# Kernel tuning notes

Measured on AMD Instinct MI355X. Metric: run time of the kernel, lower is better.

## Reference

```python
import jax, jax.numpy as jnp
import numpy as np

B, L, D = 2, 4096, 128      # batch, seq_len, d_model
ED = 2 * D                  # d_inner (expand=2) = 256
N = 16                      # d_state
K = 4                       # d_conv
R = (D + 15) // 16          # dt_rank = 8
H = 2 * D                   # mlp hidden = 256


def setup_inputs() -> dict:
    key = jax.random.key(0)
    ks = jax.random.split(key, 20)
    s = 0.05
    inp = {
        "x": jax.random.normal(ks[0], (B, L, D), dtype=jnp.float32),
        # outer block LayerNorm (norm1)
        "norm1_g": jnp.ones((D,), jnp.float32),
        "norm1_b": jnp.zeros((D,), jnp.float32),
        # MambaLayer inner LayerNorm
        "inner_g": jnp.ones((D,), jnp.float32),
        "inner_b": jnp.zeros((D,), jnp.float32),
        # Mamba params
        "in_w": jax.random.normal(ks[1], (2 * ED, D), jnp.float32) * s,      # in_proj (no bias)
        "conv_w": jax.random.normal(ks[2], (ED, 1, K), jnp.float32) * s,     # depthwise conv
        "conv_b": jax.random.normal(ks[3], (ED,), jnp.float32) * s,
        "xproj_w": jax.random.normal(ks[4], (R + 2 * N, ED), jnp.float32) * s,  # x_proj (no bias)
        "dt_w": jax.random.normal(ks[5], (ED, R), jnp.float32) * s,
        "dt_b": jax.random.normal(ks[6], (ED,), jnp.float32) * s,
        "A_log": jnp.tile(jnp.log(jnp.arange(1, N + 1, dtype=jnp.float32)), (ED, 1)),  # [ED,N]
        "Dp": jnp.ones((ED,), jnp.float32),
        "out_w": jax.random.normal(ks[7], (D, ED), jnp.float32) * s,         # out_proj (no bias)
        # MLP
        "fc1_w": jax.random.normal(ks[8], (H, D), jnp.float32) * s,
        "fc1_b": jnp.zeros((H,), jnp.float32),
        "fc2_w": jax.random.normal(ks[9], (D, H), jnp.float32) * s,
        "fc2_b": jnp.zeros((D,), jnp.float32),
    }
    return inp


def _ln(x, g, b, eps=1e-5):
    m = jnp.mean(x, axis=-1, keepdims=True)
    v = jnp.mean((x - m) ** 2, axis=-1, keepdims=True)
    return (x - m) * jax.lax.rsqrt(v + eps) * g + b


def _mamba(x, in_w, conv_w, conv_b, xproj_w, dt_w, dt_b, A_log, Dp, out_w):
    # x: [B, L, D]
    xz = jnp.einsum('bld,ed->ble', x, in_w)          # [B,L,2*ED]
    u, z = jnp.split(xz, 2, axis=-1)                 # each [B,L,ED]
    # causal depthwise conv1d over L
    u_c = jnp.transpose(u, (0, 2, 1))                # [B,ED,L]
    u_c = jax.lax.conv_general_dilated(
        u_c, conv_w, window_strides=(1,), padding=[(K - 1, 0)],
        dimension_numbers=('NCH', 'OIH', 'NCH'), feature_group_count=ED)
    u = jax.nn.silu(jnp.transpose(u_c, (0, 2, 1)) + conv_b)   # [B,L,ED]
    # input-dependent dt, B, C
    dbc = jnp.einsum('ble,re->blr', u, xproj_w)      # [B,L,R+2N]
    dt, Bm, Cm = jnp.split(dbc, [R, R + N], axis=-1)
    delta = jax.nn.softplus(jnp.einsum('blr,er->ble', dt, dt_w) + dt_b)  # [B,L,ED]
    A = -jnp.exp(A_log)                              # [ED,N]
    deltaA = jnp.exp(jnp.einsum('ble,en->blen', delta, A))               # [B,L,ED,N]
    deltaBu = jnp.einsum('ble,bln,ble->blen', delta, Bm, u)              # [B,L,ED,N]
    # selective scan over L
    def step(h, inp):
        dA, dBu, Ct = inp                            # [B,ED,N],[B,ED,N],[B,N]
        h = dA * h + dBu
        y = jnp.einsum('ben,bn->be', h, Ct)
        return h, y
    h0 = jnp.zeros((B, ED, N), u.dtype)
    xs = (jnp.transpose(deltaA, (1, 0, 2, 3)),
          jnp.transpose(deltaBu, (1, 0, 2, 3)),
          jnp.transpose(Cm, (1, 0, 2)))
    _, ys = jax.lax.scan(step, h0, xs)               # [L,B,ED]
    y = jnp.transpose(ys, (1, 0, 2)) + u * Dp        # [B,L,ED]
    y = y * jax.nn.silu(z)
    return jnp.einsum('ble,de->bld', y, out_w)       # [B,L,D]


def reference(x, norm1_g, norm1_b, inner_g, inner_b, in_w, conv_w, conv_b,
              xproj_w, dt_w, dt_b, A_log, Dp, out_w, fc1_w, fc1_b, fc2_w, fc2_b):
    # attn branch: mamba(inner_LN(norm1(x)))
    a = _mamba(_ln(_ln(x, norm1_g, norm1_b), inner_g, inner_b),
               in_w, conv_w, conv_b, xproj_w, dt_w, dt_b, A_log, Dp, out_w)
    x = x + a
    # mlp branch (note: original applies norm1 again to updated x)
    h = _ln(x, norm1_g, norm1_b)
    h = jax.nn.gelu(jnp.einsum('bld,hd->blh', h, fc1_w) + fc1_b, approximate=False)
    h = jnp.einsum('blh,dh->bld', h, fc2_w) + fc2_b
    return x + h
```

## Files before the change

kernel.cpp:

```cpp
#include <hip/hip_runtime.h>
#include <hip/hip_bf16.h>
#include <math.h>

#define BB 2
#define LL 4096
#define DD 128
#define ED 256
#define NN 16
#define KK 4
#define RR 8
#define HH 256
#define NT (BB*LL)
#define NC 128
#define LC 32

typedef __attribute__((ext_vector_type(8))) short short8;
typedef __attribute__((ext_vector_type(8))) unsigned short ushort8v;
typedef __attribute__((ext_vector_type(4))) float floatx4;

__device__ __forceinline__ unsigned short f2bf(float f) {
  unsigned int b = __builtin_bit_cast(unsigned int, f);
  b += 0x7FFFu + ((b >> 16) & 1u);
  return (unsigned short)(b >> 16);
}

__global__ __launch_bounds__(256) void cvt5_k(const float* __restrict__ a,
    const float* __restrict__ b, const float* __restrict__ c,
    const float* __restrict__ d, const float* __restrict__ e5,
    unsigned short* __restrict__ oa, unsigned short* __restrict__ ob,
    unsigned short* __restrict__ oc, unsigned short* __restrict__ od,
    unsigned short* __restrict__ oe) {
  const int i = blockIdx.x*256 + threadIdx.x;
  const float* src; unsigned short* dst; int off;
  if (i < 16384)      { src = a;  dst = oa; off = i; }
  else if (i < 24576) { src = b;  dst = ob; off = i - 16384; }
  else if (i < 32768) { src = c;  dst = oc; off = i - 24576; }
  else if (i < 40960) { src = d;  dst = od; off = i - 32768; }
  else                { src = e5; dst = oe; off = i - 40960; }
  const float4 v = ((const float4*)src)[off];
  unsigned int lo = f2bf(v.x) | ((unsigned int)f2bf(v.y) << 16);
  unsigned int hi = f2bf(v.z) | ((unsigned int)f2bf(v.w) << 16);
  ((uint2*)dst)[off] = make_uint2(lo, hi);
}

template<bool DOUBLE>
__global__ __launch_bounds__(256) void ln2_k(const float* __restrict__ x,
    const float* __restrict__ g1, const float* __restrict__ b1,
    const float* __restrict__ g2, const float* __restrict__ b2,
    unsigned short* __restrict__ out) {
  const int token = blockIdx.x*4 + (threadIdx.x >> 6);
  const int lane  = threadIdx.x & 63;
  float2 v = *(const float2*)(x + (size_t)token*DD + lane*2);

  auto wsum = [&](float s) -> float {
    s += __shfl_xor(s, 32); s += __shfl_xor(s, 16); s += __shfl_xor(s, 8);
    s += __shfl_xor(s, 4);  s += __shfl_xor(s, 2);  s += __shfl_xor(s, 1);
    return s;
  };

  float mean = wsum(v.x + v.y) * (1.f/128.f);
  float cx = v.x - mean, cy = v.y - mean;
  float var = wsum(cx*cx + cy*cy) * (1.f/128.f);
  float rs = rsqrtf(var + 1e-5f);
  const float2 g = *(const float2*)(g1 + lane*2);
  const float2 bb = *(const float2*)(b1 + lane*2);
  float yx = cx*rs*g.x + bb.x;
  float yy = cy*rs*g.y + bb.y;
  if constexpr (DOUBLE) {
    float m2 = wsum(yx + yy) * (1.f/128.f);
    float c2x = yx - m2, c2y = yy - m2;
    float v2 = wsum(c2x*c2x + c2y*c2y) * (1.f/128.f);
    float rs2 = rsqrtf(v2 + 1e-5f);
    const float2 g2v = *(const float2*)(g2 + lane*2);
    const float2 b2v = *(const float2*)(b2 + lane*2);
    yx = c2x*rs2*g2v.x + b2v.x;
    yy = c2y*rs2*g2v.y + b2v.y;
  }
  const unsigned int packed = f2bf(yx) | ((unsigned int)f2bf(yy) << 16);
  *(unsigned int*)(out + (size_t)token*DD + lane*2) = packed;
}

template<int KD, int EPI, typename OT>
__global__ __launch_bounds__(256) void gemm_bf_k(
    const unsigned short* __restrict__ A, const unsigned short* __restrict__ W,
    const float* __restrict__ bias, const float* __restrict__ res,
    OT* __restrict__ C, int Nn) {
  static_assert(KD % 128 == 0, "KD multiple of 128");
  __shared__ unsigned short As[64][136];
  __shared__ unsigned short Ws[64][136];

  const int row0 = blockIdx.y * 64;
  const int col0 = blockIdx.x * 64;
  const int tid  = threadIdx.x;
  const int wave = tid >> 6;
  const int lane = tid & 63;
  const int quad = lane >> 4;
  const int l16  = lane & 15;
  const int wm = (wave & 1) * 32;
  const int wn = (wave >> 1) * 32;
  const int lr = tid >> 2;
  const int lc = (tid & 3) * 32;

  floatx4 acc[2][2] = {};

  for (int ks0 = 0; ks0 < KD; ks0 += 128) {
    const unsigned short* Ap = A + (size_t)(row0 + lr)*KD + ks0 + lc;
    const unsigned short* Wp = W + (size_t)(col0 + lr)*KD + ks0 + lc;
    ushort8v av[4], wv[4];
    #pragma unroll
    for (int g = 0; g < 4; g++) {
      av[g] = *(const ushort8v*)(Ap + g*8);
      wv[g] = *(const ushort8v*)(Wp + g*8);
    }
    __syncthreads();
    #pragma unroll
    for (int g = 0; g < 4; g++) {
      *(ushort8v*)&As[lr][lc + g*8] = av[g];
      *(ushort8v*)&Ws[lr][lc + g*8] = wv[g];
    }
    __syncthreads();
    #pragma unroll
    for (int ks = 0; ks < 4; ks++) {
      const int ko = ks*32 + quad*8;
      short8 a0 = *(const short8*)&As[wm +      l16][ko];
      short8 a1 = *(const short8*)&As[wm + 16 + l16][ko];
      short8 b0 = *(const short8*)&Ws[wn +      l16][ko];
      short8 b1 = *(const short8*)&Ws[wn + 16 + l16][ko];
      acc[0][0] = __builtin_amdgcn_mfma_f32_16x16x32_bf16(a0, b0, acc[0][0], 0, 0, 0);
      acc[0][1] = __builtin_amdgcn_mfma_f32_16x16x32_bf16(a0, b1, acc[0][1], 0, 0, 0);
      acc[1][0] = __builtin_amdgcn_mfma_f32_16x16x32_bf16(a1, b0, acc[1][0], 0, 0, 0);
      acc[1][1] = __builtin_amdgcn_mfma_f32_16x16x32_bf16(a1, b1, acc[1][1], 0, 0, 0);
    }
  }

  #pragma unroll
  for (int i = 0; i < 2; i++) {
    #pragma unroll
    for (int j = 0; j < 2; j++) {
      const int n = col0 + wn + j*16 + l16;
      float bn = 0.f;
      if constexpr (EPI == 2 || EPI == 3) bn = bias[n];
      #pragma unroll
      for (int r = 0; r < 4; r++) {
        const int m = row0 + wm + i*16 + quad*4 + r;
        float v = acc[i][j][r];
        if constexpr (EPI == 2 || EPI == 3) v += bn;
        if constexpr (EPI == 2) v = 0.5f*v*(1.f + erff(v*0.70710678118f));
        const size_t o = (size_t)m*Nn + n;
        if constexpr (EPI == 1 || EPI == 3) v += res[o];
        if constexpr (sizeof(OT) == 2) C[o] = (OT)f2bf(v);
        else                           C[o] = v;
      }
    }
  }
}

__global__ __launch_bounds__(256) void mamba_mid_k(const float* __restrict__ xz,
    const float* __restrict__ cw, const float* __restrict__ cb,
    const unsigned short* __restrict__ xpwb, const float* __restrict__ dtw,
    const float* __restrict__ dtb, float* __restrict__ uc,
    float* __restrict__ dbc, float* __restrict__ delta) {
  __shared__ unsigned short As[32][264];
  __shared__ unsigned short Bs[64][264];
  __shared__ float sd[32][8];
  const int t0  = blockIdx.x * 32;
  const int tid = threadIdx.x;

  #pragma unroll
  for (int p = 0; p < 8; p++) {
    const int idx = p*256 + tid;
    const int row = idx >> 5;
    const int col = (idx & 31) * 8;
    ushort8v v = {};
    if (row < 40) v = *(const ushort8v*)(xpwb + row*ED + col);
    *(ushort8v*)&Bs[row][col] = v;
  }

  const int e = tid;
  const float4 w = *(const float4*)(cw + e*4);
  const float cbe = cb[e];
  float h0 = 0.f, h1 = 0.f, h2 = 0.f;
  if (t0 & 4095) {
    h0 = xz[(size_t)(t0-3)*(2*ED) + e];
    h1 = xz[(size_t)(t0-2)*(2*ED) + e];
    h2 = xz[(size_t)(t0-1)*(2*ED) + e];
  }
  #pragma unroll 4
  for (int i = 0; i < 32; i++) {
    const float cur = xz[(size_t)(t0+i)*(2*ED) + e];
    const float a = cbe + h0*w.x + h1*w.y + h2*w.z + cur*w.w;
    const float s = a / (1.f + __expf(-a));
    As[i][e] = f2bf(s);
    uc[(size_t)(t0+i)*ED + e] = s;
    h0 = h1; h1 = h2; h2 = cur;
  }
  __syncthreads();

  const int wave = tid >> 6, lane = tid & 63;
  const int quad = lane >> 4, l16 = lane & 15;
  const int mi = (wave & 1) * 16;
  const int j0 = (wave >> 1) * 2;
  floatx4 acc[2] = {};
  #pragma unroll
  for (int ks = 0; ks < 8; ks++) {
    const int ko = ks*32 + quad*8;
    short8 a  = *(const short8*)&As[mi + l16][ko];
    short8 b0 = *(const short8*)&Bs[j0*16 +      l16][ko];
    short8 b1 = *(const short8*)&Bs[j0*16 + 16 + l16][ko];
    acc[0] = __builtin_amdgcn_mfma_f32_16x16x32_bf16(a, b0, acc[0], 0, 0, 0);
    acc[1] = __builtin_amdgcn_mfma_f32_16x16x32_bf16(a, b1, acc[1], 0, 0, 0);
  }
  #pragma unroll
  for (int f = 0; f < 2; f++) {
    const int n = (j0 + f)*16 + l16;
    #pragma unroll
    for (int r = 0; r < 4; r++) {
      const int m = mi + quad*4 + r;
      const float v = acc[f][r];
      if (n < 40) dbc[(size_t)(t0 + m)*40 + n] = v;
      if (n < RR) sd[m][n] = v;
    }
  }
  __syncthreads();

  const float4 w0 = *(const float4*)(dtw + e*RR);
  const float4 w1 = *(const float4*)(dtw + e*RR + 4);
  const float db = dtb[e];
  #pragma unroll 4
  for (int t = 0; t < 32; t++) {
    const float a = db
        + sd[t][0]*w0.x + sd[t][1]*w0.y + sd[t][2]*w0.z + sd[t][3]*w0.w
        + sd[t][4]*w1.x + sd[t][5]*w1.y + sd[t][6]*w1.z + sd[t][7]*w1.w;
    delta[(size_t)(t0+t)*ED + e] = (a > 20.f) ? a : log1pf(__expf(a));
  }
}

__global__ __launch_bounds__(256) void scan1_k(const float* __restrict__ delta,
    const float* __restrict__ uc, const float* __restrict__ dbc,
    const float* __restrict__ A_log, float* __restrict__ cA,
    float* __restrict__ cH) {
  const int c = blockIdx.y, b = blockIdx.z;
  const int e  = blockIdx.x*128 + (threadIdx.x >> 1);
  const int n0 = (threadIdx.x & 1) * 8;
  const float4 a0 = *(const float4*)(A_log + e*NN + n0);
  const float4 a1 = *(const float4*)(A_log + e*NN + n0 + 4);
  float Aen[8] = {-__expf(a0.x), -__expf(a0.y), -__expf(a0.z), -__expf(a0.w),
                  -__expf(a1.x), -__expf(a1.y), -__expf(a1.z), -__expf(a1.w)};
  float h[8] = {};
  float sumd = 0.f;
  const size_t tok0 = (size_t)b*LL + (size_t)c*LC;
  for (int i = 0; i < LC; i++) {
    const size_t t = tok0 + i;
    const float dv = delta[t*ED + e];
    const float uv = uc[t*ED + e];
    const float du = dv * uv;
    const float4 B0 = *(const float4*)(dbc + t*40 + RR + n0);
    const float4 B1 = *(const float4*)(dbc + t*40 + RR + n0 + 4);
    const float Bv[8] = {B0.x,B0.y,B0.z,B0.w,B1.x,B1.y,B1.z,B1.w};
    sumd += dv;
    #pragma unroll
    for (int j = 0; j < 8; j++) {
      const float dA = __expf(dv * Aen[j]);
      h[j] = dA*h[j] + Bv[j]*du;
    }
  }
  const size_t base = (((size_t)c*BB + b)*ED + e)*NN + n0;
  *(float4*)(cA + base)     = make_float4(__expf(sumd*Aen[0]), __expf(sumd*Aen[1]),
                                          __expf(sumd*Aen[2]), __expf(sumd*Aen[3]));
  *(float4*)(cA + base + 4) = make_float4(__expf(sumd*Aen[4]), __expf(sumd*Aen[5]),
                                          __expf(sumd*Aen[6]), __expf(sumd*Aen[7]));
  *(float4*)(cH + base)     = make_float4(h[0], h[1], h[2], h[3]);
  *(float4*)(cH + base + 4) = make_float4(h[4], h[5], h[6], h[7]);
}

__global__ __launch_bounds__(256) void scan2_k(float* __restrict__ cA,
    const float* __restrict__ cH) {
  const int gt = blockIdx.x*256 + threadIdx.x;
  const int b = gt >> 12;
  const size_t base = (size_t)b*ED*NN + (gt & 4095);
  float h = 0.f;
  for (int c = 0; c < NC; c++) {
    const size_t idx = (size_t)c*(BB*ED*NN) + base;
    const float a = cA[idx], hh = cH[idx];
    cA[idx] = h;
    h = a*h + hh;
  }
}

__global__ __launch_bounds__(256) void scan3_k(const float* __restrict__ delta,
    const float* __restrict__ uc, const float* __restrict__ dbc,
    const float* __restrict__ xz, const float* __restrict__ A_log,
    const float* __restrict__ Dpv, const float* __restrict__ cP,
    unsigned short* __restrict__ ybf) {
  const int c = blockIdx.y, b = blockIdx.z;
  const int e    = blockIdx.x*128 + (threadIdx.x >> 1);
  const int half = threadIdx.x & 1;
  const int n0   = half * 8;
  const float4 a0 = *(const float4*)(A_log + e*NN + n0);
  const float4 a1 = *(const float4*)(A_log + e*NN + n0 + 4);
  float Aen[8] = {-__expf(a0.x), -__expf(a0.y), -__expf(a0.z), -__expf(a0.w),
                  -__expf(a1.x), -__expf(a1.y), -__expf(a1.z), -__expf(a1.w)};
  const float Dpe = Dpv[e];
  const size_t base = (((size_t)c*BB + b)*ED + e)*NN + n0;
  const float4 h0 = *(const float4*)(cP + base);
  const float4 h1 = *(const float4*)(cP + base + 4);
  float h[8] = {h0.x,h0.y,h0.z,h0.w,h1.x,h1.y,h1.z,h1.w};
  const size_t tok0 = (size_t)b*LL + (size_t)c*LC;
  for (int i = 0; i < LC; i++) {
    const size_t t = tok0 + i;
    const float dv = delta[t*ED + e];
    const float uv = uc[t*ED + e];
    const float du = dv * uv;
    const float4 B0 = *(const float4*)(dbc + t*40 + RR + n0);
    const float4 B1 = *(const float4*)(dbc + t*40 + RR + n0 + 4);
    const float4 C0 = *(const float4*)(dbc + t*40 + RR + NN + n0);
    const float4 C1 = *(const float4*)(dbc + t*40 + RR + NN + n0 + 4);
    const float Bv[8] = {B0.x,B0.y,B0.z,B0.w,B1.x,B1.y,B1.z,B1.w};
    const float Cv[8] = {C0.x,C0.y,C0.z,C0.w,C1.x,C1.y,C1.z,C1.w};
    float part = 0.f;
    #pragma unroll
    for (int j = 0; j < 8; j++) {
      const float dA = __expf(dv * Aen[j]);
      h[j] = dA*h[j] + Bv[j]*du;
      part += h[j]*Cv[j];
    }
    part += __shfl_xor(part, 1);
    if (half == 0) {
      const float zv = xz[t*(2*ED) + ED + e];
      const float g = zv / (1.f + __expf(-zv));
      ybf[t*ED + e] = f2bf((part + uv*Dpe) * g);
    }
  }
}

extern "C" void kernel_launch(void* const* d_in, const int* in_sizes, int n_in,
                              void* d_out, int out_size, void* d_ws, size_t ws_size,
                              hipStream_t stream) {
  const float* x      = (const float*)d_in[0];
  const float* n1g    = (const float*)d_in[1];
  const float* n1b    = (const float*)d_in[2];
  const float* ing    = (const float*)d_in[3];
  const float* inb    = (const float*)d_in[4];
  const float* in_w   = (const float*)d_in[5];
  const float* conv_w = (const float*)d_in[6];
  const float* conv_b = (const float*)d_in[7];
  const float* xproj_w= (const float*)d_in[8];
  const float* dt_w   = (const float*)d_in[9];
  const float* dt_b   = (const float*)d_in[10];
  const float* A_log  = (const float*)d_in[11];
  const float* Dpv    = (const float*)d_in[12];
  const float* out_w  = (const float*)d_in[13];
  const float* fc1_w  = (const float*)d_in[14];
  const float* fc1_b  = (const float*)d_in[15];
  const float* fc2_w  = (const float*)d_in[16];
  const float* fc2_b  = (const float*)d_in[17];
  float* out = (float*)d_out;

  float* ws    = (float*)d_ws;
  float* xz    = ws;
  float* uc    = xz    + (size_t)NT*2*ED;
  float* dbc   = uc    + (size_t)NT*ED;
  float* delta = dbc   + (size_t)NT*40;
  float* cAP   = delta + (size_t)NT*ED;
  float* cH    = cAP   + (size_t)NC*BB*ED*NN;
  float* xnew  = cH    + (size_t)NC*BB*ED*NN;
  unsigned short* xnbf  = (unsigned short*)(xnew + (size_t)NT*DD);
  unsigned short* ybf   = xnbf  + (size_t)NT*DD;
  unsigned short* hlnbf = ybf   + (size_t)NT*ED;
  unsigned short* hmlbf = hlnbf + (size_t)NT*DD;
  unsigned short* wbin  = hmlbf + (size_t)NT*HH;
  unsigned short* wbout = wbin  + (size_t)2*ED*DD;
  unsigned short* wbf1  = wbout + (size_t)DD*ED;
  unsigned short* wbf2  = wbf1  + (size_t)HH*DD;
  unsigned short* wbxp  = wbf2  + (size_t)DD*HH;

  cvt5_k<<<170, 256, 0, stream>>>(in_w, out_w, fc1_w, fc2_w, xproj_w,
                                  wbin, wbout, wbf1, wbf2, wbxp);
  ln2_k<true><<<NT/4, 256, 0, stream>>>(x, n1g, n1b, ing, inb, xnbf);
  gemm_bf_k<DD,0,float><<<dim3(512/64, NT/64), 256, 0, stream>>>(xnbf, wbin, nullptr, nullptr, xz, 2*ED);
  mamba_mid_k<<<NT/32, 256, 0, stream>>>(xz, conv_w, conv_b, wbxp, dt_w, dt_b, uc, dbc, delta);
  scan1_k<<<dim3(2, NC, BB), 256, 0, stream>>>(delta, uc, dbc, A_log, cAP, cH);
  scan2_k<<<(BB*ED*NN)/256, 256, 0, stream>>>(cAP, cH);
  scan3_k<<<dim3(2, NC, BB), 256, 0, stream>>>(delta, uc, dbc, xz, A_log, Dpv, cAP, ybf);
  gemm_bf_k<ED,1,float><<<dim3(DD/64, NT/64), 256, 0, stream>>>(ybf, wbout, nullptr, x, xnew, DD);
  ln2_k<false><<<NT/4, 256, 0, stream>>>(xnew, n1g, n1b, nullptr, nullptr, hlnbf);
  gemm_bf_k<DD,2,unsigned short><<<dim3(HH/64, NT/64), 256, 0, stream>>>(hlnbf, wbf1, fc1_b, nullptr, hmlbf, HH);
  gemm_bf_k<HH,3,float><<<dim3(DD/64, NT/64), 256, 0, stream>>>(hmlbf, wbf2, fc2_b, xnew, out, DD);
}
```

Baseline: 189.1 us.

## Fuse conv, x_proj, dt and three scan phases into one cooperative kernel

Merges the conv/x_proj/dt kernel and the three chunked-scan kernels into a single cooperative kernel that uses grid.sync between the chunk-local scan, the cross-chunk prefix and the final output pass. The conv output, delta and B/C values stay in shared memory, so the uc, dbc and delta workspace tensors are no longer written to and reread from global memory. The cross-chunk pass also batches its loads in groups of 16 to expose more memory parallelism. In exchange, each block recomputes the conv for all 256 channels, because the x_proj GEMM needs them even though the block scans only 128. The design also depends on all 512 blocks being co-resident, and the two grid-wide barriers add cost.

```diff
diff --git a/kernel.cpp b/kernel.cpp
--- a/kernel.cpp
+++ b/kernel.cpp
@@ -1,5 +1,6 @@
 #include <hip/hip_runtime.h>
 #include <hip/hip_bf16.h>
+#include <hip/hip_cooperative_groups.h>
 #include <math.h>
 
 #define BB 2
@@ -155,16 +156,28 @@
   }
 }
 
-__global__ __launch_bounds__(256) void mamba_mid_k(const float* __restrict__ xz,
-    const float* __restrict__ cw, const float* __restrict__ cb,
-    const unsigned short* __restrict__ xpwb, const float* __restrict__ dtw,
-    const float* __restrict__ dtb, float* __restrict__ uc,
-    float* __restrict__ dbc, float* __restrict__ delta) {
-  __shared__ unsigned short As[32][264];
-  __shared__ unsigned short Bs[64][264];
-  __shared__ float sd[32][8];
-  const int t0  = blockIdx.x * 32;
+__global__ __launch_bounds__(256) void mamba_core_k(
+    const float* __restrict__ xz, const float* __restrict__ cw,
+    const float* __restrict__ cb, const unsigned short* __restrict__ xpwb,
+    const float* __restrict__ dtw, const float* __restrict__ dtb,
+    const float* __restrict__ A_log, const float* __restrict__ Dpv,
+    float* __restrict__ cA, float* __restrict__ cH,
+    unsigned short* __restrict__ ybf) {
+  namespace cg = cooperative_groups;
+  cg::grid_group grid = cg::this_grid();
+
+  __shared__ __align__(16) unsigned short Bs[64][264];
+  __shared__ __align__(16) unsigned short As[32][264];
+  __shared__ float su[32][128];
+  __shared__ float sdbc[32][40];
+  float (*sdel)[128] = reinterpret_cast<float(*)[128]>(&As[0][0]);
+
+  const int gid = blockIdx.x;
+  const int eb = gid & 1;
+  const int b  = (gid >> 1) & 1;
+  const int c  = gid >> 2;
   const int tid = threadIdx.x;
+  const int t0 = b*LL + c*LC;
 
   #pragma unroll
   for (int p = 0; p < 8; p++) {
@@ -176,159 +189,154 @@
     *(ushort8v*)&Bs[row][col] = v;
   }
 
-  const int e = tid;
-  const float4 w = *(const float4*)(cw + e*4);
-  const float cbe = cb[e];
-  float h0 = 0.f, h1 = 0.f, h2 = 0.f;
-  if (t0 & 4095) {
-    h0 = xz[(size_t)(t0-3)*(2*ED) + e];
-    h1 = xz[(size_t)(t0-2)*(2*ED) + e];
-    h2 = xz[(size_t)(t0-1)*(2*ED) + e];
-  }
-  #pragma unroll 4
-  for (int i = 0; i < 32; i++) {
-    const float cur = xz[(size_t)(t0+i)*(2*ED) + e];
-    const float a = cbe + h0*w.x + h1*w.y + h2*w.z + cur*w.w;
-    const float s = a / (1.f + __expf(-a));
-    As[i][e] = f2bf(s);
-    uc[(size_t)(t0+i)*ED + e] = s;
-    h0 = h1; h1 = h2; h2 = cur;
+  {
+    const int ch = tid;
+    const float4 w = *(const float4*)(cw + ch*4);
+    const float cbe = cb[ch];
+    float h0 = 0.f, h1 = 0.f, h2 = 0.f;
+    if (c != 0) {
+      h0 = xz[(size_t)(t0-3)*(2*ED) + ch];
+      h1 = xz[(size_t)(t0-2)*(2*ED) + ch];
+      h2 = xz[(size_t)(t0-1)*(2*ED) + ch];
+    }
+    const bool own = (ch >> 7) == eb;
+    #pragma unroll 8
+    for (int i = 0; i < LC; i++) {
+      const float cur = xz[(size_t)(t0+i)*(2*ED) + ch];
+      const float a = cbe + h0*w.x + h1*w.y + h2*w.z + cur*w.w;
+      const float s = a / (1.f + __expf(-a));
+      As[i][ch] = f2bf(s);
+      if (own) su[i][ch & 127] = s;
+      h0 = h1; h1 = h2; h2 = cur;
+    }
   }
   __syncthreads();
 
   const int wave = tid >> 6, lane = tid & 63;
   const int quad = lane >> 4, l16 = lane & 15;
-  const int mi = (wave & 1) * 16;
-  const int j0 = (wave >> 1) * 2;
-  floatx4 acc[2] = {};
-  #pragma unroll
-  for (int ks = 0; ks < 8; ks++) {
-    const int ko = ks*32 + quad*8;
-    short8 a  = *(const short8*)&As[mi + l16][ko];
-    short8 b0 = *(const short8*)&Bs[j0*16 +      l16][ko];
-    short8 b1 = *(const short8*)&Bs[j0*16 + 16 + l16][ko];
-    acc[0] = __builtin_amdgcn_mfma_f32_16x16x32_bf16(a, b0, acc[0], 0, 0, 0);
-    acc[1] = __builtin_amdgcn_mfma_f32_16x16x32_bf16(a, b1, acc[1], 0, 0, 0);
-  }
-  #pragma unroll
-  for (int f = 0; f < 2; f++) {
-    const int n = (j0 + f)*16 + l16;
-    #pragma unroll
-    for (int r = 0; r < 4; r++) {
-      const int m = mi + quad*4 + r;
-      const float v = acc[f][r];
-      if (n < 40) dbc[(size_t)(t0 + m)*40 + n] = v;
-      if (n < RR) sd[m][n] = v;
+  {
+    const int mi = (wave & 1) * 16;
+    const int j0 = (wave >> 1) * 2;
+    floatx4 acc[2] = {};
+    #pragma unroll
+    for (int ks = 0; ks < 8; ks++) {
+      const int ko = ks*32 + quad*8;
+      short8 a  = *(const short8*)&As[mi + l16][ko];
+      short8 b0 = *(const short8*)&Bs[j0*16 +      l16][ko];
+      short8 b1 = *(const short8*)&Bs[j0*16 + 16 + l16][ko];
+      acc[0] = __builtin_amdgcn_mfma_f32_16x16x32_bf16(a, b0, acc[0], 0, 0, 0);
+      acc[1] = __builtin_amdgcn_mfma_f32_16x16x32_bf16(a, b1, acc[1], 0, 0, 0);
+    }
+    __syncthreads();
+    #pragma unroll
+    for (int f = 0; f < 2; f++) {
+      const int n = (j0 + f)*16 + l16;
+      #pragma unroll
+      for (int r = 0; r < 4; r++) {
+        const int m = mi + quad*4 + r;
+        if (n < 40) sdbc[m][n] = acc[f][r];
+      }
     }
   }
   __syncthreads();
 
-  const float4 w0 = *(const float4*)(dtw + e*RR);
-  const float4 w1 = *(const float4*)(dtw + e*RR + 4);
-  const float db = dtb[e];
-  #pragma unroll 4
-  for (int t = 0; t < 32; t++) {
-    const float a = db
-        + sd[t][0]*w0.x + sd[t][1]*w0.y + sd[t][2]*w0.z + sd[t][3]*w0.w
-        + sd[t][4]*w1.x + sd[t][5]*w1.y + sd[t][6]*w1.z + sd[t][7]*w1.w;
-    delta[(size_t)(t0+t)*ED + e] = (a > 20.f) ? a : log1pf(__expf(a));
-  }
-}
-
-__global__ __launch_bounds__(256) void scan1_k(const float* __restrict__ delta,
-    const float* __restrict__ uc, const float* __restrict__ dbc,
-    const float* __restrict__ A_log, float* __restrict__ cA,
-    float* __restrict__ cH) {
-  const int c = blockIdx.y, b = blockIdx.z;
-  const int e  = blockIdx.x*128 + (threadIdx.x >> 1);
-  const int n0 = (threadIdx.x & 1) * 8;
+  const int e_loc = tid >> 1;
+  const int half  = tid & 1;
+  const int e     = eb*128 + e_loc;
+  {
+    const float4 w0 = *(const float4*)(dtw + e*RR);
+    const float4 w1 = *(const float4*)(dtw + e*RR + 4);
+    const float db = dtb[e];
+    #pragma unroll 4
+    for (int i = 0; i < 16; i++) {
+      const int t = half*16 + i;
+      const float a = db
+          + sdbc[t][0]*w0.x + sdbc[t][1]*w0.y + sdbc[t][2]*w0.z + sdbc[t][3]*w0.w
+          + sdbc[t][4]*w1.x + sdbc[t][5]*w1.y + sdbc[t][6]*w1.z + sdbc[t][7]*w1.w;
+      sdel[t][e_loc] = (a > 20.f) ? a : log1pf(__expf(a));
+    }
+  }
+  __syncthreads();
+
+  const int n0 = half * 8;
   const float4 a0 = *(const float4*)(A_log + e*NN + n0);
   const float4 a1 = *(const float4*)(A_log + e*NN + n0 + 4);
   float Aen[8] = {-__expf(a0.x), -__expf(a0.y), -__expf(a0.z), -__expf(a0.w),
                   -__expf(a1.x), -__expf(a1.y), -__expf(a1.z), -__expf(a1.w)};
-  float h[8] = {};
-  float sumd = 0.f;
-  const size_t tok0 = (size_t)b*LL + (size_t)c*LC;
-  for (int i = 0; i < LC; i++) {
-    const size_t t = tok0 + i;
-    const float dv = delta[t*ED + e];
-    const float uv = uc[t*ED + e];
-    const float du = dv * uv;
-    const float4 B0 = *(const float4*)(dbc + t*40 + RR + n0);
-    const float4 B1 = *(const float4*)(dbc + t*40 + RR + n0 + 4);
-    const float Bv[8] = {B0.x,B0.y,B0.z,B0.w,B1.x,B1.y,B1.z,B1.w};
-    sumd += dv;
-    #pragma unroll
-    for (int j = 0; j < 8; j++) {
-      const float dA = __expf(dv * Aen[j]);
-      h[j] = dA*h[j] + Bv[j]*du;
-    }
-  }
   const size_t base = (((size_t)c*BB + b)*ED + e)*NN + n0;
-  *(float4*)(cA + base)     = make_float4(__expf(sumd*Aen[0]), __expf(sumd*Aen[1]),
-                                          __expf(sumd*Aen[2]), __expf(sumd*Aen[3]));
-  *(float4*)(cA + base + 4) = make_float4(__expf(sumd*Aen[4]), __expf(sumd*Aen[5]),
-                                          __expf(sumd*Aen[6]), __expf(sumd*Aen[7]));
-  *(float4*)(cH + base)     = make_float4(h[0], h[1], h[2], h[3]);
-  *(float4*)(cH + base + 4) = make_float4(h[4], h[5], h[6], h[7]);
-}
-
-__global__ __launch_bounds__(256) void scan2_k(float* __restrict__ cA,
-    const float* __restrict__ cH) {
-  const int gt = blockIdx.x*256 + threadIdx.x;
-  const int b = gt >> 12;
-  const size_t base = (size_t)b*ED*NN + (gt & 4095);
-  float h = 0.f;
-  for (int c = 0; c < NC; c++) {
-    const size_t idx = (size_t)c*(BB*ED*NN) + base;
-    const float a = cA[idx], hh = cH[idx];
-    cA[idx] = h;
-    h = a*h + hh;
-  }
-}
-
-__global__ __launch_bounds__(256) void scan3_k(const float* __restrict__ delta,
-    const float* __restrict__ uc, const float* __restrict__ dbc,
-    const float* __restrict__ xz, const float* __restrict__ A_log,
-    const float* __restrict__ Dpv, const float* __restrict__ cP,
-    unsigned short* __restrict__ ybf) {
-  const int c = blockIdx.y, b = blockIdx.z;
-  const int e    = blockIdx.x*128 + (threadIdx.x >> 1);
-  const int half = threadIdx.x & 1;
-  const int n0   = half * 8;
-  const float4 a0 = *(const float4*)(A_log + e*NN + n0);
-  const float4 a1 = *(const float4*)(A_log + e*NN + n0 + 4);
-  float Aen[8] = {-__expf(a0.x), -__expf(a0.y), -__expf(a0.z), -__expf(a0.w),
-                  -__expf(a1.x), -__expf(a1.y), -__expf(a1.z), -__expf(a1.w)};
-  const float Dpe = Dpv[e];
-  const size_t base = (((size_t)c*BB + b)*ED + e)*NN + n0;
-  const float4 h0 = *(const float4*)(cP + base);
-  const float4 h1 = *(const float4*)(cP + base + 4);
-  float h[8] = {h0.x,h0.y,h0.z,h0.w,h1.x,h1.y,h1.z,h1.w};
-  const size_t tok0 = (size_t)b*LL + (size_t)c*LC;
-  for (int i = 0; i < LC; i++) {
-    const size_t t = tok0 + i;
-    const float dv = delta[t*ED + e];
-    const float uv = uc[t*ED + e];
-    const float du = dv * uv;
-    const float4 B0 = *(const float4*)(dbc + t*40 + RR + n0);
-    const float4 B1 = *(const float4*)(dbc + t*40 + RR + n0 + 4);
-    const float4 C0 = *(const float4*)(dbc + t*40 + RR + NN + n0);
-    const float4 C1 = *(const float4*)(dbc + t*40 + RR + NN + n0 + 4);
-    const float Bv[8] = {B0.x,B0.y,B0.z,B0.w,B1.x,B1.y,B1.z,B1.w};
-    const float Cv[8] = {C0.x,C0.y,C0.z,C0.w,C1.x,C1.y,C1.z,C1.w};
-    float part = 0.f;
-    #pragma unroll
-    for (int j = 0; j < 8; j++) {
-      const float dA = __expf(dv * Aen[j]);
-      h[j] = dA*h[j] + Bv[j]*du;
-      part += h[j]*Cv[j];
-    }
-    part += __shfl_xor(part, 1);
-    if (half == 0) {
-      const float zv = xz[t*(2*ED) + ED + e];
-      const float g = zv / (1.f + __expf(-zv));
-      ybf[t*ED + e] = f2bf((part + uv*Dpe) * g);
+  {
+    float h[8] = {};
+    float sumd = 0.f;
+    for (int i = 0; i < LC; i++) {
+      const float dv = sdel[i][e_loc];
+      const float du = dv * su[i][e_loc];
+      const float4 B0 = *(const float4*)&sdbc[i][RR + n0];
+      const float4 B1 = *(const float4*)&sdbc[i][RR + n0 + 4];
+      const float Bv[8] = {B0.x,B0.y,B0.z,B0.w,B1.x,B1.y,B1.z,B1.w};
+      sumd += dv;
+      #pragma unroll
+      for (int j = 0; j < 8; j++)
+        h[j] = __expf(dv * Aen[j])*h[j] + Bv[j]*du;
+    }
+    *(float4*)(cA + base)     = make_float4(__expf(sumd*Aen[0]), __expf(sumd*Aen[1]),
+                                            __expf(sumd*Aen[2]), __expf(sumd*Aen[3]));
+    *(float4*)(cA + base + 4) = make_float4(__expf(sumd*Aen[4]), __expf(sumd*Aen[5]),
+                                            __expf(sumd*Aen[6]), __expf(sumd*Aen[7]));
+    *(float4*)(cH + base)     = make_float4(h[0], h[1], h[2], h[3]);
+    *(float4*)(cH + base + 4) = make_float4(h[4], h[5], h[6], h[7]);
+  }
+  grid.sync();
+
+  {
+    const int ft = gid*256 + tid;
+    if (ft < BB*ED*NN) {
+      const size_t rbase = (size_t)(ft >> 12)*ED*NN + (ft & 4095);
+      float h = 0.f;
+      for (int g = 0; g < NC/16; g++) {
+        float av[16], hv[16];
+        #pragma unroll
+        for (int i = 0; i < 16; i++) {
+          const size_t idx = (size_t)(g*16 + i)*(BB*ED*NN) + rbase;
+          av[i] = cA[idx]; hv[i] = cH[idx];
+        }
+        #pragma unroll
+        for (int i = 0; i < 16; i++) {
+          const size_t idx = (size_t)(g*16 + i)*(BB*ED*NN) + rbase;
+          cA[idx] = h;
+          h = av[i]*h + hv[i];
+        }
+      }
+    }
+  }
+  grid.sync();
+
+  {
+    const float Dpe = Dpv[e];
+    const float4 h0v = *(const float4*)(cA + base);
+    const float4 h1v = *(const float4*)(cA + base + 4);
+    float h[8] = {h0v.x,h0v.y,h0v.z,h0v.w,h1v.x,h1v.y,h1v.z,h1v.w};
+    for (int i = 0; i < LC; i++) {
+      const float dv = sdel[i][e_loc];
+      const float uv = su[i][e_loc];
+      const float du = dv * uv;
+      const float4 B0 = *(const float4*)&sdbc[i][RR + n0];
+      const float4 B1 = *(const float4*)&sdbc[i][RR + n0 + 4];
+      const float4 C0 = *(const float4*)&sdbc[i][RR + NN + n0];
+      const float4 C1 = *(const float4*)&sdbc[i][RR + NN + n0 + 4];
+      const float Bv[8] = {B0.x,B0.y,B0.z,B0.w,B1.x,B1.y,B1.z,B1.w};
+      const float Cv[8] = {C0.x,C0.y,C0.z,C0.w,C1.x,C1.y,C1.z,C1.w};
+      float part = 0.f;
+      #pragma unroll
+      for (int j = 0; j < 8; j++) {
+        h[j] = __expf(dv * Aen[j])*h[j] + Bv[j]*du;
+        part += h[j]*Cv[j];
+      }
+      part += __shfl_xor(part, 1);
+      if (half == 0) {
+        const float zv = xz[(size_t)(t0+i)*(2*ED) + ED + e];
+        const float g = zv / (1.f + __expf(-zv));
+        ybf[(size_t)(t0+i)*ED + e] = f2bf((part + uv*Dpe) * g);
+      }
     }
   }
 }
@@ -358,10 +366,7 @@
 
   float* ws    = (float*)d_ws;
   float* xz    = ws;
-  float* uc    = xz    + (size_t)NT*2*ED;
-  float* dbc   = uc    + (size_t)NT*ED;
-  float* delta = dbc   + (size_t)NT*40;
-  float* cAP   = delta + (size_t)NT*ED;
+  float* cAP   = xz    + (size_t)NT*2*ED;
   float* cH    = cAP   + (size_t)NC*BB*ED*NN;
   float* xnew  = cH    + (size_t)NC*BB*ED*NN;
   unsigned short* xnbf  = (unsigned short*)(xnew + (size_t)NT*DD);
@@ -378,10 +383,13 @@
                                   wbin, wbout, wbf1, wbf2, wbxp);
   ln2_k<true><<<NT/4, 256, 0, stream>>>(x, n1g, n1b, ing, inb, xnbf);
   gemm_bf_k<DD,0,float><<<dim3(512/64, NT/64), 256, 0, stream>>>(xnbf, wbin, nullptr, nullptr, xz, 2*ED);
-  mamba_mid_k<<<NT/32, 256, 0, stream>>>(xz, conv_w, conv_b, wbxp, dt_w, dt_b, uc, dbc, delta);
-  scan1_k<<<dim3(2, NC, BB), 256, 0, stream>>>(delta, uc, dbc, A_log, cAP, cH);
-  scan2_k<<<(BB*ED*NN)/256, 256, 0, stream>>>(cAP, cH);
-  scan3_k<<<dim3(2, NC, BB), 256, 0, stream>>>(delta, uc, dbc, xz, A_log, Dpv, cAP, ybf);
+  {
+    void* cargs[] = { (void*)&xz, (void*)&conv_w, (void*)&conv_b, (void*)&wbxp,
+                      (void*)&dt_w, (void*)&dt_b, (void*)&A_log, (void*)&Dpv,
+                      (void*)&cAP, (void*)&cH, (void*)&ybf };
+    hipLaunchCooperativeKernel((const void*)mamba_core_k, dim3(2*NC*BB), dim3(256),
+                               cargs, 0, stream);
+  }
   gemm_bf_k<ED,1,float><<<dim3(DD/64, NT/64), 256, 0, stream>>>(ybf, wbout, nullptr, x, xnew, DD);
   ln2_k<false><<<NT/4, 256, 0, stream>>>(xnew, n1g, n1b, nullptr, nullptr, hlnbf);
   gemm_bf_k<DD,2,unsigned short><<<dim3(HH/64, NT/64), 256, 0, stream>>>(hlnbf, wbf1, fc1_b, nullptr, hmlbf, HH);
```

Measured after the change: 315.0 us. 66.6% more time.
